# Kernel optimization log

Hardware: AMD Instinct MI355X
Metric: run time of the kernel (lower is better)

Reference implementation:

```python
import jax, jax.numpy as jnp
import numpy as np

N_NODES = 50000
N_EDGES = 800000
IN_FEAT = 128
H_FEAT = 64
NUM_HEADS = 4
NEG_SLOPE = 0.2  # DGL GATConv default LeakyReLU slope


def _gat_conv(feat, src, dst, W, attn_l, attn_r, bias, num_heads, out_feats):
    # feat: [N, Din]; W: [Din, H*F]; attn_l/attn_r: [H, F]; bias: [H*F]
    N = feat.shape[0]
    h = (feat @ W).reshape(N, num_heads, out_feats)          # [N, H, F]
    el = jnp.sum(h * attn_l, axis=-1)                        # [N, H]
    er = jnp.sum(h * attn_r, axis=-1)                        # [N, H]
    e = jax.nn.leaky_relu(el[src] + er[dst], NEG_SLOPE)      # [E, H]
    # segment softmax over incoming edges of each destination node
    m = jax.ops.segment_max(e, dst, num_segments=N)          # [N, H]
    ex = jnp.exp(e - m[dst])                                 # [E, H]
    s = jax.ops.segment_sum(ex, dst, num_segments=N)         # [N, H]
    alpha = ex / s[dst]                                      # [E, H]
    # attn_drop omitted (eval-mode deterministic reference)
    msg = h[src] * alpha[:, :, None]                         # [E, H, F]
    out = jax.ops.segment_sum(msg, dst, num_segments=N)      # [N, H, F]
    return out + bias.reshape(1, num_heads, out_feats)


def setup_inputs() -> dict:
    key = jax.random.key(0)
    ks = jax.random.split(key, 16)
    feat = jax.random.normal(ks[0], (N_NODES, IN_FEAT), dtype=jnp.float32)
    src = jax.random.randint(ks[1], (N_EDGES,), 0, N_NODES)
    dst = jax.random.randint(ks[2], (N_EDGES,), 0, N_NODES)
    sc = 0.1
    H, F = NUM_HEADS, H_FEAT
    params = {
        'W1': jax.random.normal(ks[3], (IN_FEAT, H * F), dtype=jnp.float32) * sc,
        'al1': jax.random.normal(ks[4], (H, F), dtype=jnp.float32) * sc,
        'ar1': jax.random.normal(ks[5], (H, F), dtype=jnp.float32) * sc,
        'b1': jnp.zeros((H * F,), dtype=jnp.float32),
        'W2': jax.random.normal(ks[6], (H * F, H * F), dtype=jnp.float32) * sc,
        'al2': jax.random.normal(ks[7], (H, F), dtype=jnp.float32) * sc,
        'ar2': jax.random.normal(ks[8], (H, F), dtype=jnp.float32) * sc,
        'b2': jnp.zeros((H * F,), dtype=jnp.float32),
        'W3': jax.random.normal(ks[9], (H * F, F), dtype=jnp.float32) * sc,
        'al3': jax.random.normal(ks[10], (1, F), dtype=jnp.float32) * sc,
        'ar3': jax.random.normal(ks[11], (1, F), dtype=jnp.float32) * sc,
        'b3': jnp.zeros((F,), dtype=jnp.float32),
    }
    return {'feat': feat, 'src': src, 'dst': dst, **params}


def reference(feat, src, dst, W1, al1, ar1, b1, W2, al2, ar2, b2, W3, al3, ar3, b3):
    h = _gat_conv(feat, src, dst, W1, al1, ar1, b1, NUM_HEADS, H_FEAT)
    h = jax.nn.relu(h.reshape(h.shape[0], -1))               # flatten(1) + relu
    h = _gat_conv(h, src, dst, W2, al2, ar2, b2, NUM_HEADS, H_FEAT)
    h = jax.nn.relu(h.reshape(h.shape[0], -1))
    h = _gat_conv(h, src, dst, W3, al3, ar3, b3, 1, H_FEAT)
    return h.mean(axis=1)                                    # [N, h_feat]
```

## Files before the change

### kernel.cpp

```cpp
#include <hip/hip_runtime.h>
#include <math.h>

#define N_NODES 50000
#define N_EDGES 800000

typedef short bf8 __attribute__((ext_vector_type(8)));
typedef float f4x __attribute__((ext_vector_type(4)));

__device__ __forceinline__ unsigned short f2bf(float x) {
  unsigned u = __float_as_uint(x);
  unsigned r = (u + 0x7fff + ((u >> 16) & 1)) >> 16;
  return (unsigned short)r;
}
__device__ __forceinline__ float bf2f(unsigned short b) {
  return __uint_as_float(((unsigned)b) << 16);
}
__device__ __forceinline__ unsigned pack2(float lo, float hi) {
  return (unsigned)f2bf(lo) | ((unsigned)f2bf(hi) << 16);
}

__global__ __launch_bounds__(256) void gemm_mfma_k(
    const float* __restrict__ X, const float* __restrict__ W,
    unsigned short* __restrict__ Yb, int N, int K, int M) {
  __shared__ unsigned short As[128][40];
  __shared__ unsigned short Bs[64][40];
  const int tile_n = blockIdx.x * 128;
  const int cb = blockIdx.y * 64;
  const int t = threadIdx.x;
  const int wave = t >> 6, lane = t & 63;
  const int quad = lane >> 4, l16 = lane & 15;

  f4x acc[2][4];
#pragma unroll
  for (int i = 0; i < 2; ++i)
#pragma unroll
    for (int j = 0; j < 4; ++j) acc[i][j] = (f4x){0.f, 0.f, 0.f, 0.f};

  const int ar = t >> 1;
  const int ac0 = (t & 1) * 16;
  const int bn = t & 63;
  const int bkq = t >> 6;

  for (int k0 = 0; k0 < K; k0 += 32) {
    {
      int gr = tile_n + ar;
      uint4 u0, u1;
      if (gr < N) {
        const float* s = X + (size_t)gr * K + k0 + ac0;
        float4 a = *(const float4*)(s + 0);
        float4 b = *(const float4*)(s + 4);
        float4 c = *(const float4*)(s + 8);
        float4 d = *(const float4*)(s + 12);
        u0 = make_uint4(pack2(a.x, a.y), pack2(a.z, a.w),
                        pack2(b.x, b.y), pack2(b.z, b.w));
        u1 = make_uint4(pack2(c.x, c.y), pack2(c.z, c.w),
                        pack2(d.x, d.y), pack2(d.z, d.w));
      } else {
        u0 = make_uint4(0, 0, 0, 0);
        u1 = make_uint4(0, 0, 0, 0);
      }
      *(uint4*)&As[ar][ac0] = u0;
      *(uint4*)&As[ar][ac0 + 8] = u1;
    }
    {
      const float* s = W + (size_t)(k0 + bkq * 8) * M + cb + bn;
      float w0 = s[0 * M], w1 = s[1 * M], w2 = s[2 * M], w3 = s[3 * M];
      float w4 = s[4 * M], w5 = s[5 * M], w6 = s[6 * M], w7 = s[7 * M];
      uint4 u = make_uint4(pack2(w0, w1), pack2(w2, w3), pack2(w4, w5),
                           pack2(w6, w7));
      *(uint4*)&Bs[bn][bkq * 8] = u;
    }
    __syncthreads();
    bf8 afrag[2], bfrag[4];
#pragma unroll
    for (int rt = 0; rt < 2; ++rt)
      afrag[rt] = *(const bf8*)&As[wave * 32 + rt * 16 + l16][quad * 8];
#pragma unroll
    for (int ct = 0; ct < 4; ++ct)
      bfrag[ct] = *(const bf8*)&Bs[ct * 16 + l16][quad * 8];
#pragma unroll
    for (int rt = 0; rt < 2; ++rt)
#pragma unroll
      for (int ct = 0; ct < 4; ++ct)
        acc[rt][ct] = __builtin_amdgcn_mfma_f32_16x16x32_bf16(
            afrag[rt], bfrag[ct], acc[rt][ct], 0, 0, 0);
    __syncthreads();
  }
#pragma unroll
  for (int rt = 0; rt < 2; ++rt) {
#pragma unroll
    for (int r = 0; r < 4; ++r) {
      int row = tile_n + wave * 32 + rt * 16 + quad * 4 + r;
      if (row < N) {
#pragma unroll
        for (int ct = 0; ct < 4; ++ct)
          Yb[(size_t)row * M + cb + ct * 16 + l16] = f2bf(acc[rt][ct][r]);
      }
    }
  }
}

template <int H, int F>
__global__ __launch_bounds__(256) void elr_kernel(
    const unsigned short* __restrict__ hb, const float* __restrict__ al,
    const float* __restrict__ ar, float* __restrict__ el,
    float* __restrict__ er, int N) {
  int node = blockIdx.x * 4 + (threadIdx.x >> 6);
  int lane = threadIdx.x & 63;
  if (node >= N) return;
  constexpr int V = (H * F) / 64;
  constexpr int G = F / V;
  int base = lane * V;
  int head = base / F;
  int fo = base % F;
  float sl = 0.f, sr = 0.f;
  if (V == 4) {
    ushort4 hv = *(const ushort4*)(hb + (size_t)node * H * F + base);
    float x0 = bf2f(hv.x), x1 = bf2f(hv.y), x2 = bf2f(hv.z), x3 = bf2f(hv.w);
    sl = x0 * al[head * F + fo] + x1 * al[head * F + fo + 1] +
         x2 * al[head * F + fo + 2] + x3 * al[head * F + fo + 3];
    sr = x0 * ar[head * F + fo] + x1 * ar[head * F + fo + 1] +
         x2 * ar[head * F + fo + 2] + x3 * ar[head * F + fo + 3];
  } else {
    float x = bf2f(hb[(size_t)node * H * F + base]);
    sl = x * al[head * F + fo];
    sr = x * ar[head * F + fo];
  }
#pragma unroll
  for (int off = G / 2; off > 0; off >>= 1) {
    sl += __shfl_xor(sl, off, G);
    sr += __shfl_xor(sr, off, G);
  }
  if ((lane % G) == 0) {
    el[node * H + head] = sl;
    er[node * H + head] = sr;
  }
}

__global__ __launch_bounds__(256) void count_deg_k(
    const int* __restrict__ dst, int* __restrict__ deg, int E) {
  int e = blockIdx.x * blockDim.x + threadIdx.x;
  if (e < E) atomicAdd(&deg[dst[e]], 1);
}

__global__ __launch_bounds__(256) void alloc_rows_k(
    const int* __restrict__ deg, int* __restrict__ rowstart,
    int* __restrict__ cursor, int* __restrict__ gcounter, int N) {
  int i = blockIdx.x * blockDim.x + threadIdx.x;
  int lane = threadIdx.x & 63;
  int d = (i < N) ? deg[i] : 0;
  int x = d;
#pragma unroll
  for (int off = 1; off < 64; off <<= 1) {
    int t = __shfl_up(x, off);
    if (lane >= off) x += t;
  }
  int wsum = __shfl(x, 63);
  int base = 0;
  if (lane == 63) base = atomicAdd(gcounter, wsum);
  base = __shfl(base, 63);
  if (i < N) {
    int mystart = base + x - d;
    rowstart[i] = mystart;
    cursor[i] = mystart;
  }
}

__global__ __launch_bounds__(256) void scatter_k(
    const int* __restrict__ src, const int* __restrict__ dst,
    int* __restrict__ cursor, int* __restrict__ src_sorted, int E) {
  int e = blockIdx.x * blockDim.x + threadIdx.x;
  if (e < E) {
    int p = atomicAdd(&cursor[dst[e]], 1);
    src_sorted[p] = src[e];
  }
}

template <int RELU>
__global__ __launch_bounds__(256) void node_agg4_k(
    const unsigned short* __restrict__ hb, const float* __restrict__ el,
    const float* __restrict__ er, const int* __restrict__ rowstart,
    const int* __restrict__ rowend, const int* __restrict__ src_sorted,
    float* __restrict__ albuf, const float* __restrict__ bias,
    float* __restrict__ out, int N) {
  int node = blockIdx.x * 4 + (threadIdx.x >> 6);
  int lane = threadIdx.x & 63;
  if (node >= N) {
    __syncthreads();
    return;
  }
  int start = rowstart[node], end = rowend[node];
  int head1 = lane & 3;
  int slot = lane >> 2;
  float er_v = er[node * 4 + head1];
  float m = -1e30f;
  for (int p = start + slot; p < end; p += 16) {
    int s = src_sorted[p];
    float v = el[s * 4 + head1] + er_v;
    v = (v >= 0.f) ? v : 0.2f * v;
    m = fmaxf(m, v);
  }
#pragma unroll
  for (int off = 4; off < 64; off <<= 1) m = fmaxf(m, __shfl_xor(m, off));
  float ssum = 0.f;
  for (int p = start + slot; p < end; p += 16) {
    int s = src_sorted[p];
    float v = el[s * 4 + head1] + er_v;
    v = (v >= 0.f) ? v : 0.2f * v;
    float ex = __expf(v - m);
    ssum += ex;
    albuf[p * 4 + head1] = ex;
  }
#pragma unroll
  for (int off = 4; off < 64; off <<= 1) ssum += __shfl_xor(ssum, off);
  float inv_s = (end > start) ? 1.f / ssum : 0.f;
  int hf = lane >> 4;
  float inv_f = __shfl(inv_s, hf);
  __syncthreads();
  float4 acc = make_float4(0.f, 0.f, 0.f, 0.f);
  int fo = lane << 2;
  for (int p = start; p < end; p += 4) {
    bool b1 = p + 1 < end, b2 = p + 2 < end, b3 = p + 3 < end;
    int s0 = src_sorted[p];
    int s1 = b1 ? src_sorted[p + 1] : s0;
    int s2 = b2 ? src_sorted[p + 2] : s0;
    int s3 = b3 ? src_sorted[p + 3] : s0;
    float a0 = albuf[p * 4 + hf];
    float a1 = b1 ? albuf[(p + 1) * 4 + hf] : 0.f;
    float a2 = b2 ? albuf[(p + 2) * 4 + hf] : 0.f;
    float a3 = b3 ? albuf[(p + 3) * 4 + hf] : 0.f;
    ushort4 h0 = *(const ushort4*)(hb + (size_t)s0 * 256 + fo);
    ushort4 h1 = *(const ushort4*)(hb + (size_t)s1 * 256 + fo);
    ushort4 h2 = *(const ushort4*)(hb + (size_t)s2 * 256 + fo);
    ushort4 h3 = *(const ushort4*)(hb + (size_t)s3 * 256 + fo);
    acc.x += bf2f(h0.x) * a0 + bf2f(h1.x) * a1 + bf2f(h2.x) * a2 + bf2f(h3.x) * a3;
    acc.y += bf2f(h0.y) * a0 + bf2f(h1.y) * a1 + bf2f(h2.y) * a2 + bf2f(h3.y) * a3;
    acc.z += bf2f(h0.z) * a0 + bf2f(h1.z) * a1 + bf2f(h2.z) * a2 + bf2f(h3.z) * a3;
    acc.w += bf2f(h0.w) * a0 + bf2f(h1.w) * a1 + bf2f(h2.w) * a2 + bf2f(h3.w) * a3;
  }
  const float4 b = *(const float4*)(bias + fo);
  acc.x = acc.x * inv_f + b.x;
  acc.y = acc.y * inv_f + b.y;
  acc.z = acc.z * inv_f + b.z;
  acc.w = acc.w * inv_f + b.w;
  if (RELU) {
    acc.x = fmaxf(acc.x, 0.f); acc.y = fmaxf(acc.y, 0.f);
    acc.z = fmaxf(acc.z, 0.f); acc.w = fmaxf(acc.w, 0.f);
  }
  *(float4*)(out + (size_t)node * 256 + fo) = acc;
}

__global__ __launch_bounds__(256) void node_agg1_k(
    const unsigned short* __restrict__ hb, const float* __restrict__ el,
    const float* __restrict__ er, const int* __restrict__ rowstart,
    const int* __restrict__ rowend, const int* __restrict__ src_sorted,
    float* __restrict__ albuf, const float* __restrict__ bias,
    float* __restrict__ out, int N) {
  int node = blockIdx.x * 4 + (threadIdx.x >> 6);
  int lane = threadIdx.x & 63;
  if (node >= N) {
    __syncthreads();
    return;
  }
  int start = rowstart[node], end = rowend[node];
  float er_v = er[node];
  float m = -1e30f;
  for (int p = start + lane; p < end; p += 64) {
    float v = el[src_sorted[p]] + er_v;
    v = (v >= 0.f) ? v : 0.2f * v;
    m = fmaxf(m, v);
  }
#pragma unroll
  for (int off = 1; off < 64; off <<= 1) m = fmaxf(m, __shfl_xor(m, off));
  float ssum = 0.f;
  for (int p = start + lane; p < end; p += 64) {
    float v = el[src_sorted[p]] + er_v;
    v = (v >= 0.f) ? v : 0.2f * v;
    float ex = __expf(v - m);
    ssum += ex;
    albuf[p] = ex;
  }
#pragma unroll
  for (int off = 1; off < 64; off <<= 1) ssum += __shfl_xor(ssum, off);
  float inv_s = (end > start) ? 1.f / ssum : 0.f;
  __syncthreads();
  float acc = 0.f;
  for (int p = start; p < end; p += 4) {
    bool b1 = p + 1 < end, b2 = p + 2 < end, b3 = p + 3 < end;
    int s0 = src_sorted[p];
    int s1 = b1 ? src_sorted[p + 1] : s0;
    int s2 = b2 ? src_sorted[p + 2] : s0;
    int s3 = b3 ? src_sorted[p + 3] : s0;
    float a0 = albuf[p];
    float a1 = b1 ? albuf[p + 1] : 0.f;
    float a2 = b2 ? albuf[p + 2] : 0.f;
    float a3 = b3 ? albuf[p + 3] : 0.f;
    float h0 = bf2f(hb[(size_t)s0 * 64 + lane]);
    float h1 = bf2f(hb[(size_t)s1 * 64 + lane]);
    float h2 = bf2f(hb[(size_t)s2 * 64 + lane]);
    float h3 = bf2f(hb[(size_t)s3 * 64 + lane]);
    acc += h0 * a0 + h1 * a1 + h2 * a2 + h3 * a3;
  }
  out[(size_t)node * 64 + lane] = acc * inv_s + bias[lane];
}

extern "C" void kernel_launch(void* const* d_in, const int* in_sizes, int n_in,
                              void* d_out, int out_size, void* d_ws,
                              size_t ws_size, hipStream_t stream) {
  const float* feat = (const float*)d_in[0];
  const int* src = (const int*)d_in[1];
  const int* dst = (const int*)d_in[2];
  const float* W1 = (const float*)d_in[3];
  const float* al1 = (const float*)d_in[4];
  const float* ar1 = (const float*)d_in[5];
  const float* b1 = (const float*)d_in[6];
  const float* W2 = (const float*)d_in[7];
  const float* al2 = (const float*)d_in[8];
  const float* ar2 = (const float*)d_in[9];
  const float* b2 = (const float*)d_in[10];
  const float* W3 = (const float*)d_in[11];
  const float* al3 = (const float*)d_in[12];
  const float* ar3 = (const float*)d_in[13];
  const float* b3 = (const float*)d_in[14];
  float* out = (float*)d_out;

  unsigned short* hb = (unsigned short*)d_ws;
  float* f = (float*)(hb + (size_t)N_NODES * 256);
  float* el = f + (size_t)N_NODES * 256;
  float* er = el + (size_t)N_NODES * 4;
  int* rowstart = (int*)(er + (size_t)N_NODES * 4);
  int* cursor = rowstart + N_NODES;
  int* deg = cursor + N_NODES;
  int* gcounter = deg + N_NODES;
  int* src_sorted = gcounter + 1;
  float* albuf = (float*)(src_sorted + N_EDGES);

  const int N = N_NODES, E = N_EDGES;
  const int GX = (N + 127) / 128;

  hipMemsetAsync(deg, 0, (size_t)(N + 1) * sizeof(int), stream);
  hipLaunchKernelGGL(count_deg_k, dim3((E + 255) / 256), dim3(256), 0, stream,
                     dst, deg, E);
  hipLaunchKernelGGL(alloc_rows_k, dim3((N + 255) / 256), dim3(256), 0, stream,
                     deg, rowstart, cursor, gcounter, N);
  hipLaunchKernelGGL(scatter_k, dim3((E + 255) / 256), dim3(256), 0, stream,
                     src, dst, cursor, src_sorted, E);

  hipLaunchKernelGGL(gemm_mfma_k, dim3(GX, 4), dim3(256), 0, stream, feat, W1,
                     hb, N, 128, 256);
  hipLaunchKernelGGL((elr_kernel<4, 64>), dim3((N + 3) / 4), dim3(256), 0,
                     stream, hb, al1, ar1, el, er, N);
  hipLaunchKernelGGL((node_agg4_k<1>), dim3((N + 3) / 4), dim3(256), 0, stream,
                     hb, el, er, rowstart, cursor, src_sorted, albuf, b1, f, N);

  hipLaunchKernelGGL(gemm_mfma_k, dim3(GX, 4), dim3(256), 0, stream, f, W2, hb,
                     N, 256, 256);
  hipLaunchKernelGGL((elr_kernel<4, 64>), dim3((N + 3) / 4), dim3(256), 0,
                     stream, hb, al2, ar2, el, er, N);
  hipLaunchKernelGGL((node_agg4_k<1>), dim3((N + 3) / 4), dim3(256), 0, stream,
                     hb, el, er, rowstart, cursor, src_sorted, albuf, b2, f, N);

  hipLaunchKernelGGL(gemm_mfma_k, dim3(GX, 1), dim3(256), 0, stream, f, W3, hb,
                     N, 256, 64);
  hipLaunchKernelGGL((elr_kernel<1, 64>), dim3((N + 3) / 4), dim3(256), 0,
                     stream, hb, al3, ar3, el, er, N);
  hipLaunchKernelGGL(node_agg1_k, dim3((N + 3) / 4), dim3(256), 0, stream, hb,
                     el, er, rowstart, cursor, src_sorted, albuf, b3, out, N);
}
```

Baseline: 507.0 us.

## Fuse attention logits into GEMM, drop softmax max pass, bf16 intermediates, wider gathers

Computes el/er inside the GEMM epilogue through a 16-lane shuffle reduction, which removes the separate elr kernels. Drops the segment-max pass from the softmax, so the edge list is read one fewer time. This relies on the logits being small enough that exp cannot overflow. Stores the layer activations as bf16 and feeds them to a bf16-input GEMM path, halving the intermediate traffic. The aggregation kernels now gather 16-byte vectors per lane with several edges in flight.

```diff
diff --git a/kernel.cpp b/kernel.cpp
--- a/kernel.cpp
+++ b/kernel.cpp
@@ -6,6 +6,7 @@
 
 typedef short bf8 __attribute__((ext_vector_type(8)));
 typedef float f4x __attribute__((ext_vector_type(4)));
+typedef unsigned short us8 __attribute__((ext_vector_type(8)));
 
 __device__ __forceinline__ unsigned short f2bf(float x) {
   unsigned u = __float_as_uint(x);
@@ -19,9 +20,12 @@
   return (unsigned)f2bf(lo) | ((unsigned)f2bf(hi) << 16);
 }
 
+template <int ABF16>
 __global__ __launch_bounds__(256) void gemm_mfma_k(
-    const float* __restrict__ X, const float* __restrict__ W,
-    unsigned short* __restrict__ Yb, int N, int K, int M) {
+    const void* __restrict__ Xv, const float* __restrict__ W,
+    unsigned short* __restrict__ Yb, float* __restrict__ el,
+    float* __restrict__ er, const float* __restrict__ al,
+    const float* __restrict__ ar, int N, int K, int M) {
   __shared__ unsigned short As[128][40];
   __shared__ unsigned short Bs[64][40];
   const int tile_n = blockIdx.x * 128;
@@ -36,14 +40,26 @@
 #pragma unroll
     for (int j = 0; j < 4; ++j) acc[i][j] = (f4x){0.f, 0.f, 0.f, 0.f};
 
-  const int ar = t >> 1;
+  const int ar_ = t >> 1;
   const int ac0 = (t & 1) * 16;
   const int bn = t & 63;
   const int bkq = t >> 6;
 
   for (int k0 = 0; k0 < K; k0 += 32) {
-    {
-      int gr = tile_n + ar;
+    if (ABF16) {
+      const unsigned short* Xb = (const unsigned short*)Xv;
+      int gr = tile_n + ar_;
+      us8 u0 = (us8)0, u1 = (us8)0;
+      if (gr < N) {
+        const unsigned short* s = Xb + (size_t)gr * K + k0 + ac0;
+        u0 = *(const us8*)(s + 0);
+        u1 = *(const us8*)(s + 8);
+      }
+      *(us8*)&As[ar_][ac0] = u0;
+      *(us8*)&As[ar_][ac0 + 8] = u1;
+    } else {
+      const float* X = (const float*)Xv;
+      int gr = tile_n + ar_;
       uint4 u0, u1;
       if (gr < N) {
         const float* s = X + (size_t)gr * K + k0 + ac0;
@@ -59,8 +75,8 @@
         u0 = make_uint4(0, 0, 0, 0);
         u1 = make_uint4(0, 0, 0, 0);
       }
-      *(uint4*)&As[ar][ac0] = u0;
-      *(uint4*)&As[ar][ac0 + 8] = u1;
+      *(uint4*)&As[ar_][ac0] = u0;
+      *(uint4*)&As[ar_][ac0 + 8] = u1;
     }
     {
       const float* s = W + (size_t)(k0 + bkq * 8) * M + cb + bn;
@@ -86,54 +102,37 @@
             afrag[rt], bfrag[ct], acc[rt][ct], 0, 0, 0);
     __syncthreads();
   }
+  const int H = M >> 6;
+  const int head = cb >> 6;
+  float al4[4], ar4[4];
+#pragma unroll
+  for (int ct = 0; ct < 4; ++ct) {
+    al4[ct] = al[cb + ct * 16 + l16];
+    ar4[ct] = ar[cb + ct * 16 + l16];
+  }
 #pragma unroll
   for (int rt = 0; rt < 2; ++rt) {
 #pragma unroll
     for (int r = 0; r < 4; ++r) {
       int row = tile_n + wave * 32 + rt * 16 + quad * 4 + r;
-      if (row < N) {
-#pragma unroll
-        for (int ct = 0; ct < 4; ++ct)
-          Yb[(size_t)row * M + cb + ct * 16 + l16] = f2bf(acc[rt][ct][r]);
-      }
-    }
-  }
-}
-
-template <int H, int F>
-__global__ __launch_bounds__(256) void elr_kernel(
-    const unsigned short* __restrict__ hb, const float* __restrict__ al,
-    const float* __restrict__ ar, float* __restrict__ el,
-    float* __restrict__ er, int N) {
-  int node = blockIdx.x * 4 + (threadIdx.x >> 6);
-  int lane = threadIdx.x & 63;
-  if (node >= N) return;
-  constexpr int V = (H * F) / 64;
-  constexpr int G = F / V;
-  int base = lane * V;
-  int head = base / F;
-  int fo = base % F;
-  float sl = 0.f, sr = 0.f;
-  if (V == 4) {
-    ushort4 hv = *(const ushort4*)(hb + (size_t)node * H * F + base);
-    float x0 = bf2f(hv.x), x1 = bf2f(hv.y), x2 = bf2f(hv.z), x3 = bf2f(hv.w);
-    sl = x0 * al[head * F + fo] + x1 * al[head * F + fo + 1] +
-         x2 * al[head * F + fo + 2] + x3 * al[head * F + fo + 3];
-    sr = x0 * ar[head * F + fo] + x1 * ar[head * F + fo + 1] +
-         x2 * ar[head * F + fo + 2] + x3 * ar[head * F + fo + 3];
-  } else {
-    float x = bf2f(hb[(size_t)node * H * F + base]);
-    sl = x * al[head * F + fo];
-    sr = x * ar[head * F + fo];
-  }
-#pragma unroll
-  for (int off = G / 2; off > 0; off >>= 1) {
-    sl += __shfl_xor(sl, off, G);
-    sr += __shfl_xor(sr, off, G);
-  }
-  if ((lane % G) == 0) {
-    el[node * H + head] = sl;
-    er[node * H + head] = sr;
+      float pl = 0.f, pr = 0.f;
+#pragma unroll
+      for (int ct = 0; ct < 4; ++ct) {
+        float y = acc[rt][ct][r];
+        pl += y * al4[ct];
+        pr += y * ar4[ct];
+        if (row < N) Yb[(size_t)row * M + cb + ct * 16 + l16] = f2bf(y);
+      }
+#pragma unroll
+      for (int off = 1; off < 16; off <<= 1) {
+        pl += __shfl_xor(pl, off);
+        pr += __shfl_xor(pr, off);
+      }
+      if (l16 == 0 && row < N) {
+        el[row * H + head] = pl;
+        er[row * H + head] = pr;
+      }
+    }
   }
 }
 
@@ -182,7 +181,7 @@
     const float* __restrict__ er, const int* __restrict__ rowstart,
     const int* __restrict__ rowend, const int* __restrict__ src_sorted,
     float* __restrict__ albuf, const float* __restrict__ bias,
-    float* __restrict__ out, int N) {
+    unsigned short* __restrict__ outb, int N) {
   int node = blockIdx.x * 4 + (threadIdx.x >> 6);
   int lane = threadIdx.x & 63;
   if (node >= N) {
@@ -193,61 +192,58 @@
   int head1 = lane & 3;
   int slot = lane >> 2;
   float er_v = er[node * 4 + head1];
-  float m = -1e30f;
-  for (int p = start + slot; p < end; p += 16) {
-    int s = src_sorted[p];
-    float v = el[s * 4 + head1] + er_v;
-    v = (v >= 0.f) ? v : 0.2f * v;
-    m = fmaxf(m, v);
-  }
-#pragma unroll
-  for (int off = 4; off < 64; off <<= 1) m = fmaxf(m, __shfl_xor(m, off));
   float ssum = 0.f;
   for (int p = start + slot; p < end; p += 16) {
     int s = src_sorted[p];
     float v = el[s * 4 + head1] + er_v;
     v = (v >= 0.f) ? v : 0.2f * v;
-    float ex = __expf(v - m);
+    float ex = __expf(v);
     ssum += ex;
     albuf[p * 4 + head1] = ex;
   }
 #pragma unroll
   for (int off = 4; off < 64; off <<= 1) ssum += __shfl_xor(ssum, off);
   float inv_s = (end > start) ? 1.f / ssum : 0.f;
-  int hf = lane >> 4;
-  float inv_f = __shfl(inv_s, hf);
+  int eslot = lane >> 5;
+  int flane = lane & 31;
+  int fo8 = flane << 3;
+  int headf = fo8 >> 6;
+  float inv_f = __shfl(inv_s, headf);
   __syncthreads();
-  float4 acc = make_float4(0.f, 0.f, 0.f, 0.f);
-  int fo = lane << 2;
-  for (int p = start; p < end; p += 4) {
-    bool b1 = p + 1 < end, b2 = p + 2 < end, b3 = p + 3 < end;
-    int s0 = src_sorted[p];
-    int s1 = b1 ? src_sorted[p + 1] : s0;
-    int s2 = b2 ? src_sorted[p + 2] : s0;
-    int s3 = b3 ? src_sorted[p + 3] : s0;
-    float a0 = albuf[p * 4 + hf];
-    float a1 = b1 ? albuf[(p + 1) * 4 + hf] : 0.f;
-    float a2 = b2 ? albuf[(p + 2) * 4 + hf] : 0.f;
-    float a3 = b3 ? albuf[(p + 3) * 4 + hf] : 0.f;
-    ushort4 h0 = *(const ushort4*)(hb + (size_t)s0 * 256 + fo);
-    ushort4 h1 = *(const ushort4*)(hb + (size_t)s1 * 256 + fo);
-    ushort4 h2 = *(const ushort4*)(hb + (size_t)s2 * 256 + fo);
-    ushort4 h3 = *(const ushort4*)(hb + (size_t)s3 * 256 + fo);
-    acc.x += bf2f(h0.x) * a0 + bf2f(h1.x) * a1 + bf2f(h2.x) * a2 + bf2f(h3.x) * a3;
-    acc.y += bf2f(h0.y) * a0 + bf2f(h1.y) * a1 + bf2f(h2.y) * a2 + bf2f(h3.y) * a3;
-    acc.z += bf2f(h0.z) * a0 + bf2f(h1.z) * a1 + bf2f(h2.z) * a2 + bf2f(h3.z) * a3;
-    acc.w += bf2f(h0.w) * a0 + bf2f(h1.w) * a1 + bf2f(h2.w) * a2 + bf2f(h3.w) * a3;
-  }
-  const float4 b = *(const float4*)(bias + fo);
-  acc.x = acc.x * inv_f + b.x;
-  acc.y = acc.y * inv_f + b.y;
-  acc.z = acc.z * inv_f + b.z;
-  acc.w = acc.w * inv_f + b.w;
-  if (RELU) {
-    acc.x = fmaxf(acc.x, 0.f); acc.y = fmaxf(acc.y, 0.f);
-    acc.z = fmaxf(acc.z, 0.f); acc.w = fmaxf(acc.w, 0.f);
-  }
-  *(float4*)(out + (size_t)node * 256 + fo) = acc;
+  float acc[8] = {0.f, 0.f, 0.f, 0.f, 0.f, 0.f, 0.f, 0.f};
+  for (int p0 = start; p0 < end; p0 += 8) {
+    int sj[4];
+    float aj[4];
+#pragma unroll
+    for (int j = 0; j < 4; ++j) {
+      int p = p0 + 2 * j + eslot;
+      bool v = p < end;
+      sj[j] = 0;
+      aj[j] = 0.f;
+      if (v) {
+        sj[j] = src_sorted[p];
+        aj[j] = albuf[p * 4 + headf];
+      }
+    }
+#pragma unroll
+    for (int j = 0; j < 4; ++j) {
+      us8 hv = *(const us8*)(hb + (size_t)sj[j] * 256 + fo8);
+#pragma unroll
+      for (int q = 0; q < 8; ++q) acc[q] += bf2f(hv[q]) * aj[j];
+    }
+  }
+#pragma unroll
+  for (int q = 0; q < 8; ++q) acc[q] += __shfl_xor(acc[q], 32);
+  if (eslot == 0) {
+    us8 o;
+#pragma unroll
+    for (int q = 0; q < 8; ++q) {
+      float v = acc[q] * inv_f + bias[fo8 + q];
+      if (RELU) v = fmaxf(v, 0.f);
+      o[q] = f2bf(v);
+    }
+    *(us8*)(outb + (size_t)node * 256 + fo8) = o;
+  }
 }
 
 __global__ __launch_bounds__(256) void node_agg1_k(
@@ -264,44 +260,52 @@
   }
   int start = rowstart[node], end = rowend[node];
   float er_v = er[node];
-  float m = -1e30f;
-  for (int p = start + lane; p < end; p += 64) {
-    float v = el[src_sorted[p]] + er_v;
-    v = (v >= 0.f) ? v : 0.2f * v;
-    m = fmaxf(m, v);
-  }
-#pragma unroll
-  for (int off = 1; off < 64; off <<= 1) m = fmaxf(m, __shfl_xor(m, off));
   float ssum = 0.f;
   for (int p = start + lane; p < end; p += 64) {
     float v = el[src_sorted[p]] + er_v;
     v = (v >= 0.f) ? v : 0.2f * v;
-    float ex = __expf(v - m);
+    float ex = __expf(v);
     ssum += ex;
     albuf[p] = ex;
   }
 #pragma unroll
   for (int off = 1; off < 64; off <<= 1) ssum += __shfl_xor(ssum, off);
   float inv_s = (end > start) ? 1.f / ssum : 0.f;
+  int eslot = lane >> 3;
+  int flane = lane & 7;
+  int fo8 = flane << 3;
   __syncthreads();
-  float acc = 0.f;
-  for (int p = start; p < end; p += 4) {
-    bool b1 = p + 1 < end, b2 = p + 2 < end, b3 = p + 3 < end;
-    int s0 = src_sorted[p];
-    int s1 = b1 ? src_sorted[p + 1] : s0;
-    int s2 = b2 ? src_sorted[p + 2] : s0;
-    int s3 = b3 ? src_sorted[p + 3] : s0;
-    float a0 = albuf[p];
-    float a1 = b1 ? albuf[p + 1] : 0.f;
-    float a2 = b2 ? albuf[p + 2] : 0.f;
-    float a3 = b3 ? albuf[p + 3] : 0.f;
-    float h0 = bf2f(hb[(size_t)s0 * 64 + lane]);
-    float h1 = bf2f(hb[(size_t)s1 * 64 + lane]);
-    float h2 = bf2f(hb[(size_t)s2 * 64 + lane]);
-    float h3 = bf2f(hb[(size_t)s3 * 64 + lane]);
-    acc += h0 * a0 + h1 * a1 + h2 * a2 + h3 * a3;
-  }
-  out[(size_t)node * 64 + lane] = acc * inv_s + bias[lane];
+  float acc[8] = {0.f, 0.f, 0.f, 0.f, 0.f, 0.f, 0.f, 0.f};
+  for (int p0 = start; p0 < end; p0 += 16) {
+    int sj[2];
+    float aj[2];
+#pragma unroll
+    for (int j = 0; j < 2; ++j) {
+      int p = p0 + 8 * j + eslot;
+      bool v = p < end;
+      sj[j] = 0;
+      aj[j] = 0.f;
+      if (v) {
+        sj[j] = src_sorted[p];
+        aj[j] = albuf[p];
+      }
+    }
+#pragma unroll
+    for (int j = 0; j < 2; ++j) {
+      us8 hv = *(const us8*)(hb + (size_t)sj[j] * 64 + fo8);
+#pragma unroll
+      for (int q = 0; q < 8; ++q) acc[q] += bf2f(hv[q]) * aj[j];
+    }
+  }
+#pragma unroll
+  for (int off = 8; off < 64; off <<= 1)
+#pragma unroll
+    for (int q = 0; q < 8; ++q) acc[q] += __shfl_xor(acc[q], off);
+  if (eslot == 0) {
+    float* o = out + (size_t)node * 64 + fo8;
+#pragma unroll
+    for (int q = 0; q < 8; ++q) o[q] = acc[q] * inv_s + bias[fo8 + q];
+  }
 }
 
 extern "C" void kernel_launch(void* const* d_in, const int* in_sizes, int n_in,
@@ -325,8 +329,8 @@
   float* out = (float*)d_out;
 
   unsigned short* hb = (unsigned short*)d_ws;
-  float* f = (float*)(hb + (size_t)N_NODES * 256);
-  float* el = f + (size_t)N_NODES * 256;
+  unsigned short* fb = hb + (size_t)N_NODES * 256;
+  float* el = (float*)(fb + (size_t)N_NODES * 256);
   float* er = el + (size_t)N_NODES * 4;
   int* rowstart = (int*)(er + (size_t)N_NODES * 4);
   int* cursor = rowstart + N_NODES;
@@ -346,24 +350,20 @@
   hipLaunchKernelGGL(scatter_k, dim3((E + 255) / 256), dim3(256), 0, stream,
                      src, dst, cursor, src_sorted, E);
 
-  hipLaunchKernelGGL(gemm_mfma_k, dim3(GX, 4), dim3(256), 0, stream, feat, W1,
-                     hb, N, 128, 256);
-  hipLaunchKernelGGL((elr_kernel<4, 64>), dim3((N + 3) / 4), dim3(256), 0,
-                     stream, hb, al1, ar1, el, er, N);
+  hipLaunchKernelGGL((gemm_mfma_k<0>), dim3(GX, 4), dim3(256), 0, stream, feat,
+                     W1, hb, el, er, al1, ar1, N, 128, 256);
   hipLaunchKernelGGL((node_agg4_k<1>), dim3((N + 3) / 4), dim3(256), 0, stream,
-                     hb, el, er, rowstart, cursor, src_sorted, albuf, b1, f, N);
-
-  hipLaunchKernelGGL(gemm_mfma_k, dim3(GX, 4), dim3(256), 0, stream, f, W2, hb,
-                     N, 256, 256);
-  hipLaunchKernelGGL((elr_kernel<4, 64>), dim3((N + 3) / 4), dim3(256), 0,
-                     stream, hb, al2, ar2, el, er, N);
+                     hb, el, er, rowstart, cursor, src_sorted, albuf, b1, fb,
+                     N);
+
+  hipLaunchKernelGGL((gemm_mfma_k<1>), dim3(GX, 4), dim3(256), 0, stream, fb,
+                     W2, hb, el, er, al2, ar2, N, 256, 256);
   hipLaunchKernelGGL((node_agg4_k<1>), dim3((N + 3) / 4), dim3(256), 0, stream,
-                     hb, el, er, rowstart, cursor, src_sorted, albuf, b2, f, N);
-
-  hipLaunchKernelGGL(gemm_mfma_k, dim3(GX, 1), dim3(256), 0, stream, f, W3, hb,
-                     N, 256, 64);
-  hipLaunchKernelGGL((elr_kernel<1, 64>), dim3((N + 3) / 4), dim3(256), 0,
-                     stream, hb, al3, ar3, el, er, N);
+                     hb, el, er, rowstart, cursor, src_sorted, albuf, b2, fb,
+                     N);
+
+  hipLaunchKernelGGL((gemm_mfma_k<1>), dim3(GX, 1), dim3(256), 0, stream, fb,
+                     W3, hb, el, er, al3, ar3, N, 256, 64);
   hipLaunchKernelGGL(node_agg1_k, dim3((N + 3) / 4), dim3(256), 0, stream, hb,
                      el, er, rowstart, cursor, src_sorted, albuf, b3, out, N);
 }
```

After: 425.2 us. 1.19x faster.
